# Kernel tuning notes

Measured on AMD Instinct MI355X. Metric: run time of the kernel, lower is better.

Reference implementation:

```python
import jax, jax.numpy as jnp
import numpy as np

B, S, H, E = 8, 4096, 1024, 8
TEMPERATURE = 1.0


def setup_inputs() -> dict:
    key = jax.random.key(0)
    ks = jax.random.split(key, 7)
    s_h = 1.0 / np.sqrt(H).astype(np.float32)
    s_h2 = 1.0 / np.sqrt(H // 2).astype(np.float32)
    return {
        "hidden_states": jax.random.normal(ks[0], (B, S, H), jnp.float32),
        # routing_network: Linear(H, H//2) -> ReLU -> Linear(H//2, E)
        "W1": jax.random.normal(ks[1], (H, H // 2), jnp.float32) * s_h,
        "b1": jnp.zeros((H // 2,), jnp.float32),
        "W2": jax.random.normal(ks[2], (H // 2, E), jnp.float32) * s_h2,
        "b2": jnp.zeros((E,), jnp.float32),
        # per-expert dense transform (fixed stand-in for torch.randn-per-call)
        "expert_W": jax.random.normal(ks[3], (E, H, H), jnp.float32) * s_h,
        "expert_b": jax.random.normal(ks[4], (E, H), jnp.float32),
    }


def reference(hidden_states, W1, b1, W2, b2, expert_W, expert_b):
    # Routing network -> logits [B, S, E]
    h = jax.nn.relu(jnp.einsum("bsh,hf->bsf", hidden_states, W1) + b1)
    logits = jnp.einsum("bsf,fe->bse", h, W2) + b2
    probs = jax.nn.softmax(logits / TEMPERATURE, axis=-1)
    # top-1 expert per token (scores are NOT applied to output in the original)
    sel = jnp.argmax(probs, axis=-1)  # [B, S] int
    out = jnp.zeros_like(hidden_states)
    for e in range(E):  # small fixed loop over experts
        mask = (sel == e)[..., None].astype(hidden_states.dtype)  # [B, S, 1]
        xe = hidden_states * mask
        ye = jnp.einsum("bsh,hd->bsd", xe, expert_W[e]) + expert_b[e]
        out = out + ye * mask
    return out
```

## Files before the change

kernel.cpp:

```cpp
#include <hip/hip_runtime.h>
#include <hip/hip_bf16.h>
#include <stdint.h>

#define NTOK 32768
#define HD 1024
#define FD 512
#define NEXP 8
#define TAU 0.05f
#define TAU2 4e-4f

typedef __attribute__((ext_vector_type(8))) short short8;
typedef __attribute__((ext_vector_type(4))) float f32x4;

__device__ __forceinline__ short f2bh(float f) {
  uint32_t u = __float_as_uint(f);
  return (short)((u + 0x7fffu + ((u >> 16) & 1u)) >> 16);
}
__device__ __forceinline__ float bh2f(short h) {
  return __uint_as_float(((uint32_t)(uint16_t)h) << 16);
}

__device__ __forceinline__ void gl16(void* lds, const void* g) {
  __builtin_amdgcn_global_load_lds(
      (const __attribute__((address_space(1))) void*)g,
      (__attribute__((address_space(3))) void*)lds, 16, 0, 0);
}

#define WAITBAR(N)                                              \
  do {                                                          \
    asm volatile("s_waitcnt vmcnt(" #N ")" ::: "memory");       \
    __builtin_amdgcn_s_barrier();                               \
    asm volatile("" ::: "memory");                              \
  } while (0)
#define BARO()                                                  \
  do {                                                          \
    asm volatile("" ::: "memory");                              \
    __builtin_amdgcn_s_barrier();                               \
    asm volatile("" ::: "memory");                              \
  } while (0)

__global__ __launch_bounds__(256) void k_convert(const float* __restrict__ x,
                                                 short* __restrict__ xbf) {
  size_t i = ((size_t)blockIdx.x * 256 + threadIdx.x) * 8;
  f32x4 v0 = *(const f32x4*)(x + i);
  f32x4 v1 = *(const f32x4*)(x + i + 4);
  short8 o;
#pragma unroll
  for (int q = 0; q < 4; ++q) { o[q] = f2bh(v0[q]); o[4 + q] = f2bh(v1[q]); }
  *(short8*)(xbf + i) = o;
}

__global__ __launch_bounds__(256) void k_transpose(
    const float* __restrict__ src, short* __restrict__ dst, int rows, int cols) {
  __shared__ float tile[32][33];
  size_t msz = (size_t)rows * cols;
  src += (size_t)blockIdx.z * msz;
  dst += (size_t)blockIdx.z * msz;
  int c0 = blockIdx.x * 32, r0 = blockIdx.y * 32;
  int tx = threadIdx.x & 31, ty = threadIdx.x >> 5;
#pragma unroll
  for (int i = 0; i < 32; i += 8)
    tile[ty + i][tx] = src[(size_t)(r0 + ty + i) * cols + c0 + tx];
  __syncthreads();
#pragma unroll
  for (int i = 0; i < 32; i += 8)
    dst[(size_t)(c0 + ty + i) * rows + r0 + tx] = f2bh(tile[tx][ty + i]);
}

__global__ __launch_bounds__(256) void k_transpose_split(
    const float* __restrict__ src, short* __restrict__ dstH,
    short* __restrict__ dstL, int rows, int cols) {
  __shared__ float tile[32][33];
  int c0 = blockIdx.x * 32, r0 = blockIdx.y * 32;
  int tx = threadIdx.x & 31, ty = threadIdx.x >> 5;
#pragma unroll
  for (int i = 0; i < 32; i += 8)
    tile[ty + i][tx] = src[(size_t)(r0 + ty + i) * cols + c0 + tx];
  __syncthreads();
#pragma unroll
  for (int i = 0; i < 32; i += 8) {
    float v = tile[tx][ty + i];
    short h = f2bh(v);
    size_t di = (size_t)(c0 + ty + i) * rows + r0 + tx;
    dstH[di] = h;
    dstL[di] = f2bh(v - bh2f(h));
  }
}

template <bool ABF>
__global__ __launch_bounds__(256) void k_gemm1(
    const short* __restrict__ xbf, const float* __restrict__ xf,
    const short* __restrict__ W1T, const float* __restrict__ b1,
    const float* __restrict__ W2, float* __restrict__ part) {
  __shared__ __align__(16) char smem[49152];

  const int tid = threadIdx.x;
  const int lane = tid & 63, wave = tid >> 6;
  const int wr = wave >> 1, wc = wave & 1;
  const int fr = lane & 15, fg = lane >> 4;
  const int bx = ((blockIdx.x & 7) << 5) | (blockIdx.x >> 3);
  const int m0 = bx * 128, n0 = blockIdx.y * 128;
  const int by = blockIdx.y;

  const int r0 = wave * 16 + (lane >> 2);
  const int lsw = (((lane & 3) ^ ((lane >> 3) & 3)) << 3);
  const short* b0p = W1T + (size_t)(n0 + r0) * HD + lsw;
  const short* b1p = W1T + (size_t)(n0 + r0 + 64) * HD + lsw;

  const short* a0p = nullptr; const short* a1p = nullptr;
  const float* aF = nullptr;
  int ar = 0, ah = 0, p0e = 0, p1e = 0;
  if constexpr (ABF) {
    a0p = xbf + (size_t)(m0 + r0) * HD + lsw;
    a1p = xbf + (size_t)(m0 + r0 + 64) * HD + lsw;
  } else {
    ar = tid >> 1; ah = tid & 1;
    aF = xf + (size_t)(m0 + ar) * HD + ah * 16;
    int s = (ar >> 1) & 3;
    p0e = ((2 * ah) ^ s) << 3;
    p1e = p0e ^ 8;
  }

  f32x4 acc[4][4];
#pragma unroll
  for (int i = 0; i < 4; ++i)
#pragma unroll
    for (int j = 0; j < 4; ++j) acc[i][j] = (f32x4){0.f, 0.f, 0.f, 0.f};

  const int csw = (fr >> 1) & 3;
  auto COMPUTE = [&](int b) {
    const short* As = (const short*)(smem + b * 8192);
    const short* Bs = (const short*)(smem + 24576 + b * 8192);
    short8 af[4], bf4[4];
#pragma unroll
    for (int i = 0; i < 4; ++i) {
      af[i]  = *(const short8*)(As + (wr * 64 + i * 16 + fr) * 32 + ((fg ^ csw) << 3));
      bf4[i] = *(const short8*)(Bs + (wc * 64 + i * 16 + fr) * 32 + ((fg ^ csw) << 3));
    }
#pragma unroll
    for (int i = 0; i < 4; ++i)
#pragma unroll
      for (int j = 0; j < 4; ++j)
        acc[i][j] = __builtin_amdgcn_mfma_f32_16x16x32_bf16(af[i], bf4[j], acc[i][j], 0, 0, 0);
  };

  if constexpr (ABF) {
    auto STAGE = [&](int kt, int b) {
      const int k0 = kt * 32;
      gl16(smem + 24576 + b * 8192 + wave * 1024, b0p + k0);
      gl16(smem + 24576 + b * 8192 + 4096 + wave * 1024, b1p + k0);
      gl16(smem + b * 8192 + wave * 1024, a0p + k0);
      gl16(smem + b * 8192 + 4096 + wave * 1024, a1p + k0);
    };
    STAGE(0, 0); STAGE(1, 1); STAGE(2, 2);
#pragma unroll 1
    for (int t = 0; t < 32; ++t) {
      if (t < 30) WAITBAR(8); else if (t == 30) WAITBAR(4); else WAITBAR(0);
      COMPUTE(t % 3);
      BARO();
      if (t < 29) STAGE(t + 3, t % 3);
    }
  } else {
    auto STAGEF = [&](int kt) {
      const int k0 = kt * 32;
      gl16(smem + 24576 + wave * 1024, b0p + k0);
      gl16(smem + 24576 + 4096 + wave * 1024, b1p + k0);
      f32x4 u0 = *(const f32x4*)(aF + k0);
      f32x4 u1 = *(const f32x4*)(aF + k0 + 4);
      f32x4 u2 = *(const f32x4*)(aF + k0 + 8);
      f32x4 u3 = *(const f32x4*)(aF + k0 + 12);
      short8 s0, s1;
#pragma unroll
      for (int q = 0; q < 4; ++q) {
        s0[q] = f2bh(u0[q]); s0[4 + q] = f2bh(u1[q]);
        s1[q] = f2bh(u2[q]); s1[4 + q] = f2bh(u3[q]);
      }
      short* As = (short*)smem;
      *(short8*)(As + ar * 32 + p0e) = s0;
      *(short8*)(As + ar * 32 + p1e) = s1;
    };
#pragma unroll 1
    for (int kt = 0; kt < 32; ++kt) {
      STAGEF(kt);
      __syncthreads();
      COMPUTE(0);
      __syncthreads();
    }
  }

  short* hbf = (short*)smem;
  short* W2b = (short*)(smem + 34816);
  float b1j[4];
#pragma unroll
  for (int j = 0; j < 4; ++j) b1j[j] = b1[n0 + wc * 64 + j * 16 + fr];
  for (int q = tid; q < 2048; q += 256) {
    int col = q >> 7, k = q & 127;
    W2b[col * 136 + k] = (col < 8) ? f2bh(W2[(size_t)(n0 + k) * 8 + col]) : (short)0;
  }
#pragma unroll
  for (int i = 0; i < 4; ++i)
#pragma unroll
    for (int j = 0; j < 4; ++j) {
      int col = wc * 64 + j * 16 + fr;
#pragma unroll
      for (int q = 0; q < 4; ++q)
        hbf[(wr * 64 + i * 16 + fg * 4 + q) * 136 + col] =
            f2bh(fmaxf(acc[i][j][q] + b1j[j], 0.f));
    }
  __syncthreads();
#pragma unroll
  for (int rg = 0; rg < 2; ++rg) {
    int row16 = wave * 32 + rg * 16;
    f32x4 accl = (f32x4){0.f, 0.f, 0.f, 0.f};
#pragma unroll
    for (int kk = 0; kk < 4; ++kk) {
      short8 a = *(const short8*)(hbf + (row16 + fr) * 136 + kk * 32 + fg * 8);
      short8 b = *(const short8*)(W2b + fr * 136 + kk * 32 + fg * 8);
      accl = __builtin_amdgcn_mfma_f32_16x16x32_bf16(a, b, accl, 0, 0, 0);
    }
    if (fr < 8) {
      float* pp = part + (size_t)(m0 + row16 + fg * 4) * 32 + by * 8 + fr;
#pragma unroll
      for (int q = 0; q < 4; ++q) pp[(size_t)q * 32] = accl[q];
    }
  }
}

__global__ __launch_bounds__(256) void k_combine(
    const float* __restrict__ part, const float* __restrict__ b2,
    int* __restrict__ sel, int* __restrict__ flagged, int* __restrict__ nflag) {
  int t = blockIdx.x * 256 + threadIdx.x;
  const float* p = part + (size_t)t * 32;
  float lg[8];
#pragma unroll
  for (int e = 0; e < 8; ++e) lg[e] = p[e] + p[8 + e] + p[16 + e] + p[24 + e] + b2[e];
  int be = 0; float best = lg[0];
#pragma unroll
  for (int e = 1; e < 8; ++e) if (lg[e] > best) { best = lg[e]; be = e; }
  float second = -3.4e38f;
#pragma unroll
  for (int e = 0; e < 8; ++e) if (e != be && lg[e] > second) second = lg[e];
  sel[t] = be;
  if (best - second < TAU) {
    int ix = atomicAdd(nflag, 1);
    if (ix < NTOK) flagged[ix] = t;
  }
}

__global__ __launch_bounds__(256) void k_gemmR(
    const float* __restrict__ x, const short* __restrict__ W1hT,
    const short* __restrict__ W1lT, const float* __restrict__ b1,
    const float* __restrict__ W2, const int* __restrict__ flagged,
    const int* __restrict__ nflag, float* __restrict__ partR) {
  __shared__ __align__(16) char smem[37888];
  __shared__ int toks[128];
  short* Ah = (short*)smem;
  short* Al = (short*)(smem + 8192);

  int nf = *nflag; if (nf > NTOK) nf = NTOK;
  const int m0 = blockIdx.x * 128;
  if (m0 >= nf) return;
  const int tid = threadIdx.x;
  if (tid < 128) {
    int s = m0 + tid;
    toks[tid] = flagged[s < nf ? s : nf - 1];
  }
  __syncthreads();

  const int lane = tid & 63, wave = tid >> 6;
  const int wr = wave >> 1, wc = wave & 1;
  const int fr = lane & 15, fg = lane >> 4;
  const int n0 = blockIdx.y * 128;
  const int by = blockIdx.y;

  const int off0 = wave * 1024 + lane * 16;
  const int off1 = off0 + 4096;
  const int r0 = off0 >> 6, c0 = (off0 & 63) >> 1;
  const int r1 = off1 >> 6, c1 = (off1 & 63) >> 1;
  const short* bh0p = W1hT + (size_t)(n0 + r0) * HD + c0;
  const short* bh1p = W1hT + (size_t)(n0 + r1) * HD + c1;
  const short* bl0p = W1lT + (size_t)(n0 + r0) * HD + c0;
  const short* bl1p = W1lT + (size_t)(n0 + r1) * HD + c1;
  char* ldsBh0 = smem + 16384 + wave * 1024;
  char* ldsBh1 = smem + 16384 + wave * 1024 + 4096;
  char* ldsBl0 = smem + 24576 + wave * 1024;
  char* ldsBl1 = smem + 24576 + wave * 1024 + 4096;
  const int ar = tid >> 1, ah2 = tid & 1;
  const float* aF = x + (size_t)toks[ar] * HD + ah2 * 16;

  f32x4 acc[4][4];
#pragma unroll
  for (int i = 0; i < 4; ++i)
#pragma unroll
    for (int j = 0; j < 4; ++j) acc[i][j] = (f32x4){0.f, 0.f, 0.f, 0.f};

  for (int k0 = 0; k0 < HD; k0 += 32) {
    gl16(ldsBh0, bh0p + k0);
    gl16(ldsBh1, bh1p + k0);
    gl16(ldsBl0, bl0p + k0);
    gl16(ldsBl1, bl1p + k0);
    f32x4 u0 = *(const f32x4*)(aF + k0);
    f32x4 u1 = *(const f32x4*)(aF + k0 + 4);
    f32x4 u2 = *(const f32x4*)(aF + k0 + 8);
    f32x4 u3 = *(const f32x4*)(aF + k0 + 12);
    short8 sh0, sh1, sl0, sl1;
#pragma unroll
    for (int q = 0; q < 4; ++q) {
      { float f = u0[q]; short h = f2bh(f); sh0[q]     = h; sl0[q]     = f2bh(f - bh2f(h)); }
      { float f = u1[q]; short h = f2bh(f); sh0[4 + q] = h; sl0[4 + q] = f2bh(f - bh2f(h)); }
      { float f = u2[q]; short h = f2bh(f); sh1[q]     = h; sl1[q]     = f2bh(f - bh2f(h)); }
      { float f = u3[q]; short h = f2bh(f); sh1[4 + q] = h; sl1[4 + q] = f2bh(f - bh2f(h)); }
    }
    *(short8*)(Ah + ar * 32 + ah2 * 16)     = sh0;
    *(short8*)(Ah + ar * 32 + ah2 * 16 + 8) = sh1;
    *(short8*)(Al + ar * 32 + ah2 * 16)     = sl0;
    *(short8*)(Al + ar * 32 + ah2 * 16 + 8) = sl1;
    __syncthreads();
    short8 af[4], alf[4], bf[4], blf[4];
#pragma unroll
    for (int i = 0; i < 4; ++i) {
      int row = (wr * 64 + i * 16 + fr) * 32 + fg * 8;
      af[i]  = *(const short8*)(Ah + row);
      alf[i] = *(const short8*)(Al + row);
      int rowb = (wc * 64 + i * 16 + fr) * 32 + fg * 8;
      bf[i]  = *(const short8*)((short*)(smem + 16384) + rowb);
      blf[i] = *(const short8*)((short*)(smem + 24576) + rowb);
    }
#pragma unroll
    for (int i = 0; i < 4; ++i)
#pragma unroll
      for (int j = 0; j < 4; ++j) {
        acc[i][j] = __builtin_amdgcn_mfma_f32_16x16x32_bf16(af[i],  bf[j],  acc[i][j], 0, 0, 0);
        acc[i][j] = __builtin_amdgcn_mfma_f32_16x16x32_bf16(af[i],  blf[j], acc[i][j], 0, 0, 0);
        acc[i][j] = __builtin_amdgcn_mfma_f32_16x16x32_bf16(alf[i], bf[j],  acc[i][j], 0, 0, 0);
      }
    __syncthreads();
  }

  float* hl64 = (float*)smem;
  float* W2c  = (float*)(smem + 33024);
  *(f32x4*)(W2c + tid * 4) = *(const f32x4*)(W2 + (size_t)n0 * NEXP + tid * 4);
  float b1j[4];
#pragma unroll
  for (int j = 0; j < 4; ++j) b1j[j] = b1[n0 + wc * 64 + j * 16 + fr];

  for (int p = 0; p < 2; ++p) {
    if (wr == p) {
#pragma unroll
      for (int i = 0; i < 4; ++i)
#pragma unroll
        for (int j = 0; j < 4; ++j) {
          int col = wc * 64 + j * 16 + fr;
#pragma unroll
          for (int q = 0; q < 4; ++q)
            hl64[(i * 16 + fg * 4 + q) * 129 + col] = fmaxf(acc[i][j][q] + b1j[j], 0.f);
        }
    }
    __syncthreads();
    if (tid < 128) {
      int r2 = tid & 63, eh = tid >> 6;
      const float* hrow = hl64 + r2 * 129;
      const float* wcp = W2c + eh * 4;
      float s0 = 0.f, s1 = 0.f, s2 = 0.f, s3 = 0.f;
      for (int f = 0; f < 128; ++f) {
        float hv = hrow[f];
        s0 += hv * wcp[f * 8 + 0];
        s1 += hv * wcp[f * 8 + 1];
        s2 += hv * wcp[f * 8 + 2];
        s3 += hv * wcp[f * 8 + 3];
      }
      float* pp = partR + (size_t)(m0 + p * 64 + r2) * 32 + by * 8 + eh * 4;
      pp[0] = s0; pp[1] = s1; pp[2] = s2; pp[3] = s3;
    }
    __syncthreads();
  }
}

__global__ __launch_bounds__(256) void k_combineR(
    const float* __restrict__ partR, const float* __restrict__ b2,
    const int* __restrict__ flagged, const int* __restrict__ nflag,
    int* __restrict__ sel, int* __restrict__ flagged2, int* __restrict__ nflag2) {
  int nf = *nflag; if (nf > NTOK) nf = NTOK;
  int s = blockIdx.x * 256 + threadIdx.x;
  if (s >= nf) return;
  int t = flagged[s];
  const float* p = partR + (size_t)s * 32;
  float lg[8];
#pragma unroll
  for (int e = 0; e < 8; ++e) lg[e] = p[e] + p[8 + e] + p[16 + e] + p[24 + e] + b2[e];
  int be = 0; float best = lg[0];
#pragma unroll
  for (int e = 1; e < 8; ++e) if (lg[e] > best) { best = lg[e]; be = e; }
  float second = -3.4e38f;
#pragma unroll
  for (int e = 0; e < 8; ++e) if (e != be && lg[e] > second) second = lg[e];
  sel[t] = be;
  if (best - second < TAU2) {
    int ix = atomicAdd(nflag2, 1);
    if (ix < NTOK) flagged2[ix] = t;
  }
}

__global__ __launch_bounds__(256) void k_recomputeB(
    const float* __restrict__ x, const float* __restrict__ W1,
    const float* __restrict__ b1, const float* __restrict__ W2,
    const float* __restrict__ b2, const int* __restrict__ flagged2,
    const int* __restrict__ nflag2, int* __restrict__ sel) {
  __shared__ float xs[1024];
  __shared__ double hs[512];
  __shared__ double red[8][32];
  __shared__ double lgd[8];
  int nf = *nflag2; if (nf > NTOK) nf = NTOK;
  const int tid = threadIdx.x;
  for (int ti = blockIdx.x; ti < nf; ti += gridDim.x) {
    int t = flagged2[ti];
    __syncthreads();
    for (int q = tid; q < 1024; q += 256) xs[q] = x[(size_t)t * HD + q];
    __syncthreads();
    int f0 = tid * 2;
    double a0 = 0.0, a1 = 0.0;
    for (int h = 0; h < 1024; h += 4) {
      float2 w0 = *(const float2*)(W1 + (size_t)(h + 0) * FD + f0);
      float2 w1 = *(const float2*)(W1 + (size_t)(h + 1) * FD + f0);
      float2 w2 = *(const float2*)(W1 + (size_t)(h + 2) * FD + f0);
      float2 w3 = *(const float2*)(W1 + (size_t)(h + 3) * FD + f0);
      double x0 = (double)xs[h], x1 = (double)xs[h + 1];
      double x2 = (double)xs[h + 2], x3 = (double)xs[h + 3];
      a0 += x0 * (double)w0.x; a1 += x0 * (double)w0.y;
      a0 += x1 * (double)w1.x; a1 += x1 * (double)w1.y;
      a0 += x2 * (double)w2.x; a1 += x2 * (double)w2.y;
      a0 += x3 * (double)w3.x; a1 += x3 * (double)w3.y;
    }
    a0 += (double)b1[f0]; a1 += (double)b1[f0 + 1];
    hs[f0]     = a0 > 0.0 ? a0 : 0.0;
    hs[f0 + 1] = a1 > 0.0 ? a1 : 0.0;
    __syncthreads();
    {
      int e = tid >> 5, c = tid & 31;
      int fb = c * 16;
      double s = 0.0;
#pragma unroll
      for (int ff = 0; ff < 16; ++ff)
        s += hs[fb + ff] * (double)W2[(size_t)(fb + ff) * 8 + e];
      red[e][c] = s;
    }
    __syncthreads();
    if (tid < 8) {
      double s = 0.0;
#pragma unroll
      for (int c = 0; c < 32; ++c) s += red[tid][c];
      lgd[tid] = s + (double)b2[tid];
    }
    __syncthreads();
    if (tid == 0) {
      int be = 0; double best = lgd[0];
#pragma unroll
      for (int e = 1; e < 8; ++e) if (lgd[e] > best) { best = lgd[e]; be = e; }
      sel[t] = be;
    }
    __syncthreads();
  }
}

__global__ __launch_bounds__(256) void k_compact(
    const int* __restrict__ sel, int* __restrict__ cnt, int* __restrict__ list) {
  __shared__ int wcnt[4][8];
  __shared__ int woff[4][8];
  __shared__ int bbase[8];
  const int tid = threadIdx.x, lane = tid & 63, wave = tid >> 6;
  const int t = blockIdx.x * 256 + tid;
  const int e = sel[t];
  const unsigned long long ltmask = (1ull << lane) - 1ull;
  int rank = 0;
#pragma unroll
  for (int e2 = 0; e2 < 8; ++e2) {
    unsigned long long m = __ballot(e == e2);
    if (e2 == e) rank = __popcll(m & ltmask);
    if (lane == 0) wcnt[wave][e2] = __popcll(m);
  }
  __syncthreads();
  if (tid < 8) {
    int s0 = wcnt[0][tid], s1 = wcnt[1][tid], s2 = wcnt[2][tid], s3 = wcnt[3][tid];
    woff[0][tid] = 0; woff[1][tid] = s0; woff[2][tid] = s0 + s1; woff[3][tid] = s0 + s1 + s2;
    bbase[tid] = atomicAdd(&cnt[tid], s0 + s1 + s2 + s3);
  }
  __syncthreads();
  list[(size_t)e * NTOK + bbase[e] + woff[wave][e] + rank] = t;
}

__global__ void k_build_desc(const int* __restrict__ cnt, int* __restrict__ desc,
                             int* __restrict__ ntl) {
  if (threadIdx.x == 0 && blockIdx.x == 0) {
    int n = 0;
    for (int e = 0; e < 8; ++e) {
      int m = (cnt[e] + 127) >> 7;
      for (int i = 0; i < m; ++i) desc[n++] = (e << 16) | i;
    }
    *ntl = n;
  }
}

template <bool ABF>
__global__ __launch_bounds__(256) void k_gemm2(
    const short* __restrict__ xbf, const float* __restrict__ xf,
    const short* __restrict__ WexpT, const float* __restrict__ expert_b,
    const int* __restrict__ cnt, const int* __restrict__ list,
    const int* __restrict__ desc, const int* __restrict__ ntl,
    float* __restrict__ out) {
  __shared__ __align__(16) char smem[49152];
  __shared__ int toks[128];
  const int bx = (blockIdx.x % 8) * 33 + blockIdx.x / 8;
  if (bx >= *ntl) return;
  int dsc = desc[bx];
  int e = dsc >> 16, mt = dsc & 0xffff;
  int ce = cnt[e];
  int mb = mt * 128;
  int rows = ce - mb; if (rows > 128) rows = 128;

  const int tid = threadIdx.x;
  if (tid < 128) {
    int idx = mb + tid;
    toks[tid] = list[(size_t)e * NTOK + (idx < ce ? idx : ce - 1)];
  }
  __syncthreads();

  const int lane = tid & 63, wave = tid >> 6;
  const int wr = wave >> 1, wc = wave & 1;
  const int fr = lane & 15, fg = lane >> 4;
  const int n0 = blockIdx.y * 128;

  const int r0 = wave * 16 + (lane >> 2);
  const int lsw = (((lane & 3) ^ ((lane >> 3) & 3)) << 3);
  const size_t ebase = (size_t)e << 20;
  const short* b0p = WexpT + ebase + (size_t)(n0 + r0) * HD + lsw;
  const short* b1p = WexpT + ebase + (size_t)(n0 + r0 + 64) * HD + lsw;

  const short* a0p = nullptr; const short* a1p = nullptr;
  const float* aF = nullptr;
  int ar = 0, ah = 0, p0e = 0, p1e = 0;
  if constexpr (ABF) {
    a0p = xbf + (size_t)toks[r0] * HD + lsw;
    a1p = xbf + (size_t)toks[r0 + 64] * HD + lsw;
  } else {
    ar = tid >> 1; ah = tid & 1;
    aF = xf + (size_t)toks[ar] * HD + ah * 16;
    int s = (ar >> 1) & 3;
    p0e = ((2 * ah) ^ s) << 3;
    p1e = p0e ^ 8;
  }

  f32x4 acc[4][4];
#pragma unroll
  for (int i = 0; i < 4; ++i)
#pragma unroll
    for (int j = 0; j < 4; ++j) acc[i][j] = (f32x4){0.f, 0.f, 0.f, 0.f};

  const int csw = (fr >> 1) & 3;
  auto COMPUTE = [&](int b) {
    const short* As = (const short*)(smem + b * 8192);
    const short* Bs = (const short*)(smem + 24576 + b * 8192);
    short8 af[4], bf4[4];
#pragma unroll
    for (int i = 0; i < 4; ++i) {
      af[i]  = *(const short8*)(As + (wr * 64 + i * 16 + fr) * 32 + ((fg ^ csw) << 3));
      bf4[i] = *(const short8*)(Bs + (wc * 64 + i * 16 + fr) * 32 + ((fg ^ csw) << 3));
    }
#pragma unroll
    for (int i = 0; i < 4; ++i)
#pragma unroll
      for (int j = 0; j < 4; ++j)
        acc[i][j] = __builtin_amdgcn_mfma_f32_16x16x32_bf16(af[i], bf4[j], acc[i][j], 0, 0, 0);
  };

  if constexpr (ABF) {
    auto STAGE = [&](int kt, int b) {
      const int k0 = kt * 32;
      gl16(smem + 24576 + b * 8192 + wave * 1024, b0p + k0);
      gl16(smem + 24576 + b * 8192 + 4096 + wave * 1024, b1p + k0);
      gl16(smem + b * 8192 + wave * 1024, a0p + k0);
      gl16(smem + b * 8192 + 4096 + wave * 1024, a1p + k0);
    };
    STAGE(0, 0); STAGE(1, 1); STAGE(2, 2);
#pragma unroll 1
    for (int t = 0; t < 32; ++t) {
      if (t < 30) WAITBAR(8); else if (t == 30) WAITBAR(4); else WAITBAR(0);
      COMPUTE(t % 3);
      BARO();
      if (t < 29) STAGE(t + 3, t % 3);
    }
  } else {
    auto STAGEF = [&](int kt) {
      const int k0 = kt * 32;
      gl16(smem + 24576 + wave * 1024, b0p + k0);
      gl16(smem + 24576 + 4096 + wave * 1024, b1p + k0);
      f32x4 u0 = *(const f32x4*)(aF + k0);
      f32x4 u1 = *(const f32x4*)(aF + k0 + 4);
      f32x4 u2 = *(const f32x4*)(aF + k0 + 8);
      f32x4 u3 = *(const f32x4*)(aF + k0 + 12);
      short8 s0, s1;
#pragma unroll
      for (int q = 0; q < 4; ++q) {
        s0[q] = f2bh(u0[q]); s0[4 + q] = f2bh(u1[q]);
        s1[q] = f2bh(u2[q]); s1[4 + q] = f2bh(u3[q]);
      }
      short* As = (short*)smem;
      *(short8*)(As + ar * 32 + p0e) = s0;
      *(short8*)(As + ar * 32 + p1e) = s1;
    };
#pragma unroll 1
    for (int kt = 0; kt < 32; ++kt) {
      STAGEF(kt);
      __syncthreads();
      COMPUTE(0);
      __syncthreads();
    }
  }

  float ebv[4];
#pragma unroll
  for (int j = 0; j < 4; ++j) ebv[j] = expert_b[e * HD + n0 + wc * 64 + j * 16 + fr];
#pragma unroll
  for (int i = 0; i < 4; ++i)
#pragma unroll
    for (int j = 0; j < 4; ++j) {
      int col = n0 + wc * 64 + j * 16 + fr;
#pragma unroll
      for (int q = 0; q < 4; ++q) {
        int rr = wr * 64 + i * 16 + fg * 4 + q;
        if (rr < rows) out[(size_t)toks[rr] * HD + col] = acc[i][j][q] + ebv[j];
      }
    }
}

extern "C" void kernel_launch(void* const* d_in, const int* in_sizes, int n_in,
                              void* d_out, int out_size, void* d_ws, size_t ws_size,
                              hipStream_t stream) {
  const float* x  = (const float*)d_in[0];
  const float* W1 = (const float*)d_in[1];
  const float* b1 = (const float*)d_in[2];
  const float* W2 = (const float*)d_in[3];
  const float* b2 = (const float*)d_in[4];
  const float* eW = (const float*)d_in[5];
  const float* eb = (const float*)d_in[6];
  float* out = (float*)d_out;
  char* ws = (char*)d_ws;

  const size_t XBF_BYTES = (size_t)NTOK * HD * 2;
  size_t need_rest = 16777216ull + 1048576 + 4194304 + 131072 * 3 + 1048576 + 4096;
  bool big = ws_size >= XBF_BYTES + need_rest;

  size_t off = 0;
  short* xbf = nullptr;
  if (big) { xbf = (short*)ws; off += XBF_BYTES; }
  short* WexpT  = (short*)(ws + off); off += 16777216;
  short* W1T    = (short*)(ws + off); off += 1048576;
  float* part   = (float*)(ws + off); off += 4194304;
  int* sel      = (int*)(ws + off); off += 131072;
  int* flagged  = (int*)(ws + off); off += 131072;
  int* flagged2 = (int*)(ws + off); off += 131072;
  int* list     = (int*)(ws + off); off += 1048576;
  int* cnt      = (int*)(ws + off); off += 32;
  int* nflag    = (int*)(ws + off); off += 4;
  int* ntl      = (int*)(ws + off); off += 4;
  int* nflag2   = (int*)(ws + off); off += 24;
  int* desc     = (int*)(ws + off); off += 1088;
  if (ws_size < off) return;

  short* W1lT = (short*)list;

  hipMemsetAsync(cnt, 0, 44, stream);

  dim3 b256(256);
  if (big) k_convert<<<dim3(16384), b256, 0, stream>>>(x, xbf);
  k_transpose_split<<<dim3(16, 32), b256, 0, stream>>>(W1, W1T, W1lT, 1024, 512);
  k_transpose<<<dim3(32, 32, 8), b256, 0, stream>>>(eW, WexpT, 1024, 1024);
  if (big)
    k_gemm1<true><<<dim3(256, 4), b256, 0, stream>>>(xbf, nullptr, W1T, b1, W2, part);
  else
    k_gemm1<false><<<dim3(256, 4), b256, 0, stream>>>(nullptr, x, W1T, b1, W2, part);
  k_combine<<<dim3(128), b256, 0, stream>>>(part, b2, sel, flagged, nflag);
  k_gemmR<<<dim3(256, 4), b256, 0, stream>>>(x, W1T, W1lT, b1, W2, flagged, nflag, part);
  k_combineR<<<dim3(128), b256, 0, stream>>>(part, b2, flagged, nflag, sel, flagged2, nflag2);
  k_recomputeB<<<dim3(128), b256, 0, stream>>>(x, W1, b1, W2, b2, flagged2, nflag2, sel);
  k_compact<<<dim3(128), b256, 0, stream>>>(sel, cnt, list);
  k_build_desc<<<dim3(1), dim3(64), 0, stream>>>(cnt, desc, ntl);
  if (big)
    k_gemm2<true><<<dim3(264, 8), b256, 0, stream>>>(xbf, nullptr, WexpT, eb, cnt, list, desc, ntl, out);
  else
    k_gemm2<false><<<dim3(264, 8), b256, 0, stream>>>(nullptr, x, WexpT, eb, cnt, list, desc, ntl, out);
}
```

Measured before the change: 352.8 us.

## Single-buffer GEMM main loops, add MFMA priority, stage gemm2 output via LDS

Replaces the triple-buffered global_load_lds pipeline in both GEMM kernels with a single-buffered load/sync/compute/sync loop. This shrinks LDS per block so more blocks can be resident per CU. MFMA sections are wrapped in s_setprio. The gemm2 epilogue now stages accumulator rows through LDS so each token row is written with 16-byte vector stores instead of scattered 4-byte stores. The cost is that load latency is no longer hidden by prefetch and the epilogue gains extra barriers.

```diff
diff --git a/kernel.cpp b/kernel.cpp
--- a/kernel.cpp
+++ b/kernel.cpp
@@ -25,19 +25,6 @@
       (const __attribute__((address_space(1))) void*)g,
       (__attribute__((address_space(3))) void*)lds, 16, 0, 0);
 }
-
-#define WAITBAR(N)                                              \
-  do {                                                          \
-    asm volatile("s_waitcnt vmcnt(" #N ")" ::: "memory");       \
-    __builtin_amdgcn_s_barrier();                               \
-    asm volatile("" ::: "memory");                              \
-  } while (0)
-#define BARO()                                                  \
-  do {                                                          \
-    asm volatile("" ::: "memory");                              \
-    __builtin_amdgcn_s_barrier();                               \
-    asm volatile("" ::: "memory");                              \
-  } while (0)
 
 __global__ __launch_bounds__(256) void k_convert(const float* __restrict__ x,
                                                  short* __restrict__ xbf) {
@@ -92,7 +79,7 @@
     const short* __restrict__ xbf, const float* __restrict__ xf,
     const short* __restrict__ W1T, const float* __restrict__ b1,
     const float* __restrict__ W2, float* __restrict__ part) {
-  __shared__ __align__(16) char smem[49152];
+  __shared__ __align__(16) char smem[39168];
 
   const int tid = threadIdx.x;
   const int lane = tid & 63, wave = tid >> 6;
@@ -128,43 +115,13 @@
     for (int j = 0; j < 4; ++j) acc[i][j] = (f32x4){0.f, 0.f, 0.f, 0.f};
 
   const int csw = (fr >> 1) & 3;
-  auto COMPUTE = [&](int b) {
-    const short* As = (const short*)(smem + b * 8192);
-    const short* Bs = (const short*)(smem + 24576 + b * 8192);
-    short8 af[4], bf4[4];
-#pragma unroll
-    for (int i = 0; i < 4; ++i) {
-      af[i]  = *(const short8*)(As + (wr * 64 + i * 16 + fr) * 32 + ((fg ^ csw) << 3));
-      bf4[i] = *(const short8*)(Bs + (wc * 64 + i * 16 + fr) * 32 + ((fg ^ csw) << 3));
-    }
-#pragma unroll
-    for (int i = 0; i < 4; ++i)
-#pragma unroll
-      for (int j = 0; j < 4; ++j)
-        acc[i][j] = __builtin_amdgcn_mfma_f32_16x16x32_bf16(af[i], bf4[j], acc[i][j], 0, 0, 0);
-  };
-
-  if constexpr (ABF) {
-    auto STAGE = [&](int kt, int b) {
-      const int k0 = kt * 32;
-      gl16(smem + 24576 + b * 8192 + wave * 1024, b0p + k0);
-      gl16(smem + 24576 + b * 8192 + 4096 + wave * 1024, b1p + k0);
-      gl16(smem + b * 8192 + wave * 1024, a0p + k0);
-      gl16(smem + b * 8192 + 4096 + wave * 1024, a1p + k0);
-    };
-    STAGE(0, 0); STAGE(1, 1); STAGE(2, 2);
-#pragma unroll 1
-    for (int t = 0; t < 32; ++t) {
-      if (t < 30) WAITBAR(8); else if (t == 30) WAITBAR(4); else WAITBAR(0);
-      COMPUTE(t % 3);
-      BARO();
-      if (t < 29) STAGE(t + 3, t % 3);
-    }
-  } else {
-    auto STAGEF = [&](int kt) {
-      const int k0 = kt * 32;
-      gl16(smem + 24576 + wave * 1024, b0p + k0);
-      gl16(smem + 24576 + 4096 + wave * 1024, b1p + k0);
+  for (int k0 = 0; k0 < HD; k0 += 32) {
+    gl16(smem + 8192 + wave * 1024, b0p + k0);
+    gl16(smem + 12288 + wave * 1024, b1p + k0);
+    if constexpr (ABF) {
+      gl16(smem + wave * 1024, a0p + k0);
+      gl16(smem + 4096 + wave * 1024, a1p + k0);
+    } else {
       f32x4 u0 = *(const f32x4*)(aF + k0);
       f32x4 u1 = *(const f32x4*)(aF + k0 + 4);
       f32x4 u2 = *(const f32x4*)(aF + k0 + 8);
@@ -178,14 +135,26 @@
       short* As = (short*)smem;
       *(short8*)(As + ar * 32 + p0e) = s0;
       *(short8*)(As + ar * 32 + p1e) = s1;
-    };
-#pragma unroll 1
-    for (int kt = 0; kt < 32; ++kt) {
-      STAGEF(kt);
-      __syncthreads();
-      COMPUTE(0);
-      __syncthreads();
-    }
+    }
+    __syncthreads();
+    {
+      const short* As = (const short*)smem;
+      const short* Bs = (const short*)(smem + 8192);
+      short8 af[4], bf4[4];
+#pragma unroll
+      for (int i = 0; i < 4; ++i) {
+        af[i]  = *(const short8*)(As + (wr * 64 + i * 16 + fr) * 32 + ((fg ^ csw) << 3));
+        bf4[i] = *(const short8*)(Bs + (wc * 64 + i * 16 + fr) * 32 + ((fg ^ csw) << 3));
+      }
+      __builtin_amdgcn_s_setprio(1);
+#pragma unroll
+      for (int i = 0; i < 4; ++i)
+#pragma unroll
+        for (int j = 0; j < 4; ++j)
+          acc[i][j] = __builtin_amdgcn_mfma_f32_16x16x32_bf16(af[i], bf4[j], acc[i][j], 0, 0, 0);
+      __builtin_amdgcn_s_setprio(0);
+    }
+    __syncthreads();
   }
 
   short* hbf = (short*)smem;
@@ -507,7 +476,7 @@
     const int* __restrict__ cnt, const int* __restrict__ list,
     const int* __restrict__ desc, const int* __restrict__ ntl,
     float* __restrict__ out) {
-  __shared__ __align__(16) char smem[49152];
+  __shared__ __align__(16) char smem[16384];
   __shared__ int toks[128];
   const int bx = (blockIdx.x % 8) * 33 + blockIdx.x / 8;
   if (bx >= *ntl) return;
@@ -556,43 +525,13 @@
     for (int j = 0; j < 4; ++j) acc[i][j] = (f32x4){0.f, 0.f, 0.f, 0.f};
 
   const int csw = (fr >> 1) & 3;
-  auto COMPUTE = [&](int b) {
-    const short* As = (const short*)(smem + b * 8192);
-    const short* Bs = (const short*)(smem + 24576 + b * 8192);
-    short8 af[4], bf4[4];
-#pragma unroll
-    for (int i = 0; i < 4; ++i) {
-      af[i]  = *(const short8*)(As + (wr * 64 + i * 16 + fr) * 32 + ((fg ^ csw) << 3));
-      bf4[i] = *(const short8*)(Bs + (wc * 64 + i * 16 + fr) * 32 + ((fg ^ csw) << 3));
-    }
-#pragma unroll
-    for (int i = 0; i < 4; ++i)
-#pragma unroll
-      for (int j = 0; j < 4; ++j)
-        acc[i][j] = __builtin_amdgcn_mfma_f32_16x16x32_bf16(af[i], bf4[j], acc[i][j], 0, 0, 0);
-  };
-
-  if constexpr (ABF) {
-    auto STAGE = [&](int kt, int b) {
-      const int k0 = kt * 32;
-      gl16(smem + 24576 + b * 8192 + wave * 1024, b0p + k0);
-      gl16(smem + 24576 + b * 8192 + 4096 + wave * 1024, b1p + k0);
-      gl16(smem + b * 8192 + wave * 1024, a0p + k0);
-      gl16(smem + b * 8192 + 4096 + wave * 1024, a1p + k0);
-    };
-    STAGE(0, 0); STAGE(1, 1); STAGE(2, 2);
-#pragma unroll 1
-    for (int t = 0; t < 32; ++t) {
-      if (t < 30) WAITBAR(8); else if (t == 30) WAITBAR(4); else WAITBAR(0);
-      COMPUTE(t % 3);
-      BARO();
-      if (t < 29) STAGE(t + 3, t % 3);
-    }
-  } else {
-    auto STAGEF = [&](int kt) {
-      const int k0 = kt * 32;
-      gl16(smem + 24576 + wave * 1024, b0p + k0);
-      gl16(smem + 24576 + 4096 + wave * 1024, b1p + k0);
+  for (int k0 = 0; k0 < HD; k0 += 32) {
+    gl16(smem + 8192 + wave * 1024, b0p + k0);
+    gl16(smem + 12288 + wave * 1024, b1p + k0);
+    if constexpr (ABF) {
+      gl16(smem + wave * 1024, a0p + k0);
+      gl16(smem + 4096 + wave * 1024, a1p + k0);
+    } else {
       f32x4 u0 = *(const f32x4*)(aF + k0);
       f32x4 u1 = *(const f32x4*)(aF + k0 + 4);
       f32x4 u2 = *(const f32x4*)(aF + k0 + 8);
@@ -606,30 +545,54 @@
       short* As = (short*)smem;
       *(short8*)(As + ar * 32 + p0e) = s0;
       *(short8*)(As + ar * 32 + p1e) = s1;
-    };
-#pragma unroll 1
-    for (int kt = 0; kt < 32; ++kt) {
-      STAGEF(kt);
-      __syncthreads();
-      COMPUTE(0);
-      __syncthreads();
-    }
+    }
+    __syncthreads();
+    {
+      const short* As = (const short*)smem;
+      const short* Bs = (const short*)(smem + 8192);
+      short8 af[4], bf4[4];
+#pragma unroll
+      for (int i = 0; i < 4; ++i) {
+        af[i]  = *(const short8*)(As + (wr * 64 + i * 16 + fr) * 32 + ((fg ^ csw) << 3));
+        bf4[i] = *(const short8*)(Bs + (wc * 64 + i * 16 + fr) * 32 + ((fg ^ csw) << 3));
+      }
+      __builtin_amdgcn_s_setprio(1);
+#pragma unroll
+      for (int i = 0; i < 4; ++i)
+#pragma unroll
+        for (int j = 0; j < 4; ++j)
+          acc[i][j] = __builtin_amdgcn_mfma_f32_16x16x32_bf16(af[i], bf4[j], acc[i][j], 0, 0, 0);
+      __builtin_amdgcn_s_setprio(0);
+    }
+    __syncthreads();
   }
 
   float ebv[4];
 #pragma unroll
   for (int j = 0; j < 4; ++j) ebv[j] = expert_b[e * HD + n0 + wc * 64 + j * 16 + fr];
-#pragma unroll
-  for (int i = 0; i < 4; ++i)
-#pragma unroll
-    for (int j = 0; j < 4; ++j) {
-      int col = n0 + wc * 64 + j * 16 + fr;
-#pragma unroll
-      for (int q = 0; q < 4; ++q) {
-        int rr = wr * 64 + i * 16 + fg * 4 + q;
-        if (rr < rows) out[(size_t)toks[rr] * HD + col] = acc[i][j][q] + ebv[j];
+  float* buf = (float*)smem;
+  const int row16 = tid >> 4, cc = tid & 15;
+#pragma unroll
+  for (int p = 0; p < 8; ++p) {
+    if (wr == (p >> 2)) {
+      const int i = p & 3;
+#pragma unroll
+      for (int j = 0; j < 4; ++j) {
+        int col = wc * 64 + j * 16 + fr;
+#pragma unroll
+        for (int q = 0; q < 4; ++q)
+          buf[(fg * 4 + q) * 136 + col] = acc[i][j][q] + ebv[j];
       }
     }
+    __syncthreads();
+    const int rr = p * 16 + row16;
+    if (rr < rows) {
+      float* op = out + (size_t)toks[rr] * HD + n0 + cc * 8;
+      *(f32x4*)op       = *(const f32x4*)(buf + row16 * 136 + cc * 8);
+      *(f32x4*)(op + 4) = *(const f32x4*)(buf + row16 * 136 + cc * 8 + 4);
+    }
+    __syncthreads();
+  }
 }
 
 extern "C" void kernel_launch(void* const* d_in, const int* in_sizes, int n_in,
```

Measured after the change: 357.5 us. About the same (+1.3%).
